# Kernel optimization log

Hardware: AMD Instinct MI355X
Metric: run time of the kernel (lower is better)

## Reference

```python
import jax, jax.numpy as jnp
import numpy as np

IN_CHS = 128
NUM_HEADS = 4
WIN = 7
N = WIN * WIN            # 49 tokens per window
QKDIM = 128              # ceil(in_chs/num_groups/num_heads)*num_heads
HEAD_DIM = QKDIM // NUM_HEADS
SCALE = HEAD_DIM ** -0.5
B = 4096                 # batch * num_windows


def _relative_position_index(win_h, win_w):
    coords = np.stack(np.meshgrid(np.arange(win_h), np.arange(win_w), indexing='ij'))  # [2,h,w]
    cf = coords.reshape(2, -1)                      # [2, N]
    rc = (cf[:, :, None] - cf[:, None, :]).transpose(1, 2, 0).astype(np.int64)  # [N,N,2]
    rc[:, :, 0] += win_h - 1
    rc[:, :, 1] += win_w - 1
    rc[:, :, 0] *= 2 * win_w - 1
    return rc.sum(-1)                               # [N, N]


def setup_inputs() -> dict:
    key = jax.random.key(0)
    ks = jax.random.split(key, 8)
    x = jax.random.normal(ks[0], (B, N, IN_CHS), dtype=jnp.float32)
    qk_w = jax.random.normal(ks[1], (2 * QKDIM, IN_CHS), dtype=jnp.float32) * 0.02
    qk_b = jnp.zeros((2 * QKDIM,), dtype=jnp.float32)
    v_w = jax.random.normal(ks[2], (IN_CHS, IN_CHS), dtype=jnp.float32) * 0.02
    v_b = jnp.zeros((IN_CHS,), dtype=jnp.float32)
    proj_w = jax.random.normal(ks[3], (IN_CHS, IN_CHS), dtype=jnp.float32) * 0.02
    proj_b = jnp.zeros((IN_CHS,), dtype=jnp.float32)
    bias_table = jax.random.normal(ks[4], ((2 * WIN - 1) * (2 * WIN - 1), NUM_HEADS), dtype=jnp.float32) * 0.02
    rel_idx = jnp.asarray(_relative_position_index(WIN, WIN))  # [N,N] int64
    return {"x": x, "qk_w": qk_w, "qk_b": qk_b, "v_w": v_w, "v_b": v_b,
            "proj_w": proj_w, "proj_b": proj_b, "bias_table": bias_table,
            "rel_idx": rel_idx}


def reference(x, qk_w, qk_b, v_w, v_b, proj_w, proj_b, bias_table, rel_idx):
    Bn, Nn, C = x.shape
    # fused q/k projection: [B,N,2*qkdim] -> q,k each [B,H,N,d]
    qk = (x @ qk_w.T + qk_b).reshape(Bn, Nn, 2, NUM_HEADS, HEAD_DIM)
    q = qk[:, :, 0].transpose(0, 2, 1, 3)
    k = qk[:, :, 1].transpose(0, 2, 1, 3)
    v = (x @ v_w.T + v_b).reshape(Bn, Nn, NUM_HEADS, -1).transpose(0, 2, 1, 3)
    # windowed QK^T with gathered relative-position bias
    attn = jnp.einsum('bhnd,bhmd->bhnm', q * SCALE, k)
    bias = bias_table[rel_idx.reshape(-1)].reshape(Nn, Nn, NUM_HEADS).transpose(2, 0, 1)
    attn = jax.nn.softmax(attn + bias[None], axis=-1)
    out = jnp.einsum('bhnm,bhmd->bhnd', attn, v).transpose(0, 2, 1, 3).reshape(Bn, Nn, -1)
    return out @ proj_w.T + proj_b
```

## Files before the change

### kernel.cpp

```cpp
#include <hip/hip_runtime.h>
#include <hip/hip_bf16.h>

typedef __attribute__((ext_vector_type(8))) __bf16 bf16x8;
typedef __attribute__((ext_vector_type(4))) short short4v;
typedef __attribute__((ext_vector_type(4))) float f32x4;

#define MFMA(a,b,c) __builtin_amdgcn_mfma_f32_16x16x32_bf16((a),(b),(c),0,0,0)
#define MFMA16(a,b,c) __builtin_amdgcn_mfma_f32_16x16x16bf16_1k((a),(b),(c),0,0,0)

#define XB 0u
#define QB 16384u
#define KB 32768u
#define VT 49152u

static __device__ __forceinline__ unsigned short f2u(float x) {
  return __builtin_bit_cast(unsigned short, static_cast<__bf16>(x));
}
static __device__ __forceinline__ unsigned long long pack4(float a, float b, float c, float d) {
  union { __bf16 h[4]; unsigned long long u; } z;
  z.h[0] = static_cast<__bf16>(a);
  z.h[1] = static_cast<__bf16>(b);
  z.h[2] = static_cast<__bf16>(c);
  z.h[3] = static_cast<__bf16>(d);
  return z.u;
}
static __device__ __forceinline__ unsigned long long pack4v(f32x4 v) {
  return pack4(v[0], v[1], v[2], v[3]);
}
static __device__ __forceinline__ short4v pack4s(float a, float b, float c, float d) {
  union { __bf16 h[4]; short4v s; } z;
  z.h[0] = static_cast<__bf16>(a);
  z.h[1] = static_cast<__bf16>(b);
  z.h[2] = static_cast<__bf16>(c);
  z.h[3] = static_cast<__bf16>(d);
  return z.s;
}
static __device__ __forceinline__ unsigned sw256(unsigned row, unsigned colb) {
  return (row << 8) + (colb ^ ((row & 7u) << 4));
}
static __device__ __forceinline__ unsigned sw128(unsigned row, unsigned colb) {
  return (row << 7) + (colb ^ ((row & 7u) << 4));
}

__global__ void rsa_prep(const float* __restrict__ qk_w, const float* __restrict__ v_w,
                         const float* __restrict__ proj_w, const float* __restrict__ bias_table,
                         unsigned short* __restrict__ wqk, unsigned short* __restrict__ wv,
                         unsigned short* __restrict__ wp, float* __restrict__ biasNN) {
  const float SCALE = 0.17677669529663687f;
  int t = blockIdx.x * blockDim.x + threadIdx.x;
  int stride = gridDim.x * blockDim.x;
  for (int i = t; i < 256 * 128; i += stride) {
    float v = qk_w[i];
    if (i < 128 * 128) v *= SCALE;
    wqk[i] = f2u(v);
  }
  for (int i = t; i < 128 * 128; i += stride) wv[i] = f2u(v_w[i]);
  for (int i = t; i < 128 * 128; i += stride) wp[i] = f2u(proj_w[i]);
  for (int i = t; i < 4 * 64 * 64; i += stride) {
    int h = i >> 12, r = (i >> 6) & 63, m = i & 63;
    float v = -1e9f;
    if (r < 49 && m < 49) {
      int ri = r / 7, rj = r - ri * 7, mi = m / 7, mj = m - mi * 7;
      int rel = (ri - mi + 6) * 13 + (rj - mj + 6);
      v = bias_table[rel * 4 + h];
    }
    biasNN[i] = v;
  }
}

__global__ __launch_bounds__(512, 4) void rsa_main(
    const float* __restrict__ x, const float* __restrict__ qk_bias,
    const float* __restrict__ v_bias, const float* __restrict__ proj_bias,
    const unsigned short* __restrict__ wqk, const unsigned short* __restrict__ wv,
    const unsigned short* __restrict__ wp, const float* __restrict__ biasNN,
    float* __restrict__ out) {
  __shared__ __align__(16) unsigned char LDS[65536];
  const int tid = threadIdx.x;
  const int w = tid >> 6;
  const int lane = tid & 63;
  const int c = lane & 15;
  const int g = lane >> 4;
  const int b = blockIdx.x;
  const float SCALE = 0.17677669529663687f;

  {
    const f32x4* xp = reinterpret_cast<const f32x4*>(x + (size_t)b * 6272);
    for (int i = tid; i < 1568; i += 512) {
      f32x4 v = xp[i];
      unsigned row = (unsigned)i >> 5, c4 = (unsigned)i & 31u;
      *reinterpret_cast<unsigned long long*>(LDS + XB + sw256(row, c4 * 8)) = pack4v(v);
    }
    for (int i = tid; i < 480; i += 512) {
      unsigned row = 49 + ((unsigned)i >> 5), c4 = (unsigned)i & 31u;
      *reinterpret_cast<unsigned long long*>(LDS + XB + sw256(row, c4 * 8)) = 0ull;
    }
  }
  __syncthreads();

  __builtin_amdgcn_s_setprio(1);
#pragma unroll
  for (int mi = 0; mi < 2; ++mi) {
    const int mt = w + 8 * mi;
    bf16x8 a[4];
    const unsigned short* wrow = wqk + (mt * 16 + c) * 128 + g * 8;
#pragma unroll
    for (int ks = 0; ks < 4; ++ks) a[ks] = *reinterpret_cast<const bf16x8*>(wrow + ks * 32);
    const int chout = mt * 16 + g * 4;
    f32x4 bias4 = *reinterpret_cast<const f32x4*>(qk_bias + chout);
    if (mi == 0) { bias4[0] *= SCALE; bias4[1] *= SCALE; bias4[2] *= SCALE; bias4[3] *= SCALE; }
#pragma unroll
    for (int nt = 0; nt < 4; ++nt) {
      f32x4 acc = {0.f, 0.f, 0.f, 0.f};
#pragma unroll
      for (int ks = 0; ks < 4; ++ks) {
        bf16x8 bf = *reinterpret_cast<const bf16x8*>(LDS + XB + sw256(nt * 16 + c, (ks * 32 + g * 8) * 2));
        acc = MFMA(a[ks], bf, acc);
      }
      const unsigned tok = nt * 16 + c;
      const unsigned colb = ((mt & 7) * 16 + g * 4) * 2;
      const unsigned base = (mi == 0) ? QB : KB;
      *reinterpret_cast<unsigned long long*>(LDS + base + sw256(tok, colb)) =
          pack4(acc[0] + bias4[0], acc[1] + bias4[1], acc[2] + bias4[2], acc[3] + bias4[3]);
    }
  }

  {
    const float vb = v_bias[w * 16 + c];
    bf16x8 bw[4];
    const unsigned short* wrow = wv + (w * 16 + c) * 128 + g * 8;
#pragma unroll
    for (int ks = 0; ks < 4; ++ks) bw[ks] = *reinterpret_cast<const bf16x8*>(wrow + ks * 32);
#pragma unroll
    for (int mt = 0; mt < 4; ++mt) {
      f32x4 acc = {0.f, 0.f, 0.f, 0.f};
#pragma unroll
      for (int ks = 0; ks < 4; ++ks) {
        bf16x8 af = *reinterpret_cast<const bf16x8*>(LDS + XB + sw256(mt * 16 + c, (ks * 32 + g * 8) * 2));
        acc = MFMA(af, bw[ks], acc);
      }
      const unsigned row = w * 16 + c;
      const unsigned colb = (mt * 16 + g * 4) * 2;
      *reinterpret_cast<unsigned long long*>(LDS + VT + sw128(row, colb)) =
          pack4(acc[0] + vb, acc[1] + vb, acc[2] + vb, acc[3] + vb);
    }
  }
  __builtin_amdgcn_s_setprio(0);
  __syncthreads();

  const int h = w >> 1;
  const int rt0 = (w & 1) * 2;

  f32x4 bb[2][4];
#pragma unroll
  for (int r2 = 0; r2 < 2; ++r2) {
    const int r = (rt0 + r2) * 16 + c;
    const float* bp = biasNN + ((h * 64 + r) << 6);
#pragma unroll
    for (int mt = 0; mt < 4; ++mt)
      bb[r2][mt] = *reinterpret_cast<const f32x4*>(bp + mt * 16 + g * 4);
  }

  f32x4 s[2][4];
  __builtin_amdgcn_s_setprio(1);
#pragma unroll
  for (int r2 = 0; r2 < 2; ++r2) {
    const int rt = rt0 + r2;
    bf16x8 qf = *reinterpret_cast<const bf16x8*>(LDS + QB + sw256(rt * 16 + c, h * 64 + g * 16));
#pragma unroll
    for (int mt = 0; mt < 4; ++mt) {
      bf16x8 kf = *reinterpret_cast<const bf16x8*>(LDS + KB + sw256(mt * 16 + c, h * 64 + g * 16));
      f32x4 z = {0.f, 0.f, 0.f, 0.f};
      s[r2][mt] = MFMA(kf, qf, z);
    }
  }
  __builtin_amdgcn_s_setprio(0);

  short4v pk[2][4];
#pragma unroll
  for (int r2 = 0; r2 < 2; ++r2) {
    float v[16];
    float sum = 0.f;
#pragma unroll
    for (int mt = 0; mt < 4; ++mt) {
#pragma unroll
      for (int j = 0; j < 4; ++j) {
        v[mt * 4 + j] = __expf(s[r2][mt][j] + bb[r2][mt][j]);
        sum += v[mt * 4 + j];
      }
    }
    sum += __shfl_xor(sum, 16);
    sum += __shfl_xor(sum, 32);
    const float inv = (sum > 0.f) ? 1.0f / sum : 0.f;
#pragma unroll
    for (int mt = 0; mt < 4; ++mt)
      pk[r2][mt] = pack4s(v[mt * 4] * inv, v[mt * 4 + 1] * inv,
                          v[mt * 4 + 2] * inv, v[mt * 4 + 3] * inv);
  }

  f32x4 od[2][2];
  {
    short4v vfrag[2][4];
#pragma unroll
    for (int ct2 = 0; ct2 < 2; ++ct2)
#pragma unroll
      for (int ks = 0; ks < 4; ++ks)
        vfrag[ct2][ks] = *reinterpret_cast<const short4v*>(
            LDS + VT + sw128((h * 2 + ct2) * 16 + c, (ks * 16 + g * 4) * 2));
    __builtin_amdgcn_s_setprio(1);
#pragma unroll
    for (int ct2 = 0; ct2 < 2; ++ct2)
#pragma unroll
      for (int r2 = 0; r2 < 2; ++r2) {
        f32x4 acc = {0.f, 0.f, 0.f, 0.f};
#pragma unroll
        for (int ks = 0; ks < 4; ++ks) acc = MFMA16(vfrag[ct2][ks], pk[r2][ks], acc);
        od[ct2][r2] = acc;
      }
    __builtin_amdgcn_s_setprio(0);
  }

  bf16x8 ap[4];
  {
    const unsigned short* wrow = wp + (w * 16 + c) * 128 + g * 8;
#pragma unroll
    for (int ks = 0; ks < 4; ++ks) ap[ks] = *reinterpret_cast<const bf16x8*>(wrow + ks * 32);
  }
  f32x4 pb4 = *reinterpret_cast<const f32x4*>(proj_bias + w * 16 + g * 4);

#pragma unroll
  for (int ct2 = 0; ct2 < 2; ++ct2)
#pragma unroll
    for (int r2 = 0; r2 < 2; ++r2) {
      const int r = (rt0 + r2) * 16 + c;
      *reinterpret_cast<unsigned long long*>(
          LDS + XB + sw256(r, ((h * 2 + ct2) * 16 + g * 4) * 2)) = pack4v(od[ct2][r2]);
    }
  __syncthreads();

  {
    __builtin_amdgcn_s_setprio(1);
#pragma unroll
    for (int nt = 0; nt < 4; ++nt) {
      f32x4 acc = {0.f, 0.f, 0.f, 0.f};
#pragma unroll
      for (int ks = 0; ks < 4; ++ks) {
        bf16x8 bf = *reinterpret_cast<const bf16x8*>(LDS + XB + sw256(nt * 16 + c, (ks * 32 + g * 8) * 2));
        acc = MFMA(ap[ks], bf, acc);
      }
      const int tok = nt * 16 + c;
      if (tok < 49) {
        f32x4 o = {acc[0] + pb4[0], acc[1] + pb4[1], acc[2] + pb4[2], acc[3] + pb4[3]};
        *reinterpret_cast<f32x4*>(out + ((size_t)b * 49 + tok) * 128 + w * 16 + g * 4) = o;
      }
    }
    __builtin_amdgcn_s_setprio(0);
  }
}

extern "C" void kernel_launch(void* const* d_in, const int* in_sizes, int n_in,
                              void* d_out, int out_size, void* d_ws, size_t ws_size,
                              hipStream_t stream) {
  const float* x          = (const float*)d_in[0];
  const float* qk_w       = (const float*)d_in[1];
  const float* qk_b       = (const float*)d_in[2];
  const float* v_w        = (const float*)d_in[3];
  const float* v_b        = (const float*)d_in[4];
  const float* proj_w     = (const float*)d_in[5];
  const float* proj_b     = (const float*)d_in[6];
  const float* bias_table = (const float*)d_in[7];
  float* out = (float*)d_out;

  unsigned short* wqk = (unsigned short*)d_ws;
  unsigned short* wv  = wqk + 256 * 128;
  unsigned short* wp  = wv + 128 * 128;
  float* biasNN = (float*)((char*)d_ws + 131072);

  const int B = in_sizes[0] / (49 * 128);

  rsa_prep<<<dim3(128), dim3(512), 0, stream>>>(qk_w, v_w, proj_w, bias_table, wqk, wv, wp, biasNN);
  rsa_main<<<dim3(B), dim3(512), 0, stream>>>(x, qk_b, v_b, proj_b, wqk, wv, wp, biasNN, out);
}
```

Before: 119.2 us.

## Process four windows per block with register-prefetched next-window input

Measured after the change: 171.2 us. 1.44x slower.

```diff
diff --git a/kernel.cpp b/kernel.cpp
--- a/kernel.cpp
+++ b/kernel.cpp
@@ -12,6 +12,8 @@
 #define QB 16384u
 #define KB 32768u
 #define VT 49152u
+#define OB 65536u
+#define NW 4
 
 static __device__ __forceinline__ unsigned short f2u(float x) {
   return __builtin_bit_cast(unsigned short, static_cast<__bf16>(x));
@@ -41,17 +43,23 @@
 static __device__ __forceinline__ unsigned sw128(unsigned row, unsigned colb) {
   return (row << 7) + (colb ^ ((row & 7u) << 4));
 }
+template <typename T>
+static __device__ __forceinline__ const T* opq(const T* p) {
+  asm volatile("" : "+s"(p));
+  return p;
+}
 
 __global__ void rsa_prep(const float* __restrict__ qk_w, const float* __restrict__ v_w,
                          const float* __restrict__ proj_w, const float* __restrict__ bias_table,
                          unsigned short* __restrict__ wqk, unsigned short* __restrict__ wv,
                          unsigned short* __restrict__ wp, float* __restrict__ biasNN) {
-  const float SCALE = 0.17677669529663687f;
+  const float QSCALE = 0.17677669529663687f * 1.4426950408889634f;
+  const float LOG2E = 1.4426950408889634f;
   int t = blockIdx.x * blockDim.x + threadIdx.x;
   int stride = gridDim.x * blockDim.x;
   for (int i = t; i < 256 * 128; i += stride) {
     float v = qk_w[i];
-    if (i < 128 * 128) v *= SCALE;
+    if (i < 128 * 128) v *= QSCALE;
     wqk[i] = f2u(v);
   }
   for (int i = t; i < 128 * 128; i += stride) wv[i] = f2u(v_w[i]);
@@ -62,7 +70,7 @@
     if (r < 49 && m < 49) {
       int ri = r / 7, rj = r - ri * 7, mi = m / 7, mj = m - mi * 7;
       int rel = (ri - mi + 6) * 13 + (rj - mj + 6);
-      v = bias_table[rel * 4 + h];
+      v = bias_table[rel * 4 + h] * LOG2E;
     }
     biasNN[i] = v;
   }
@@ -73,187 +81,209 @@
     const float* __restrict__ v_bias, const float* __restrict__ proj_bias,
     const unsigned short* __restrict__ wqk, const unsigned short* __restrict__ wv,
     const unsigned short* __restrict__ wp, const float* __restrict__ biasNN,
-    float* __restrict__ out) {
-  __shared__ __align__(16) unsigned char LDS[65536];
+    float* __restrict__ out, int Btot) {
+  __shared__ __align__(16) unsigned char LDS[81920];
   const int tid = threadIdx.x;
   const int w = tid >> 6;
   const int lane = tid & 63;
   const int c = lane & 15;
   const int g = lane >> 4;
-  const int b = blockIdx.x;
-  const float SCALE = 0.17677669529663687f;
-
-  {
-    const f32x4* xp = reinterpret_cast<const f32x4*>(x + (size_t)b * 6272);
-    for (int i = tid; i < 1568; i += 512) {
-      f32x4 v = xp[i];
-      unsigned row = (unsigned)i >> 5, c4 = (unsigned)i & 31u;
-      *reinterpret_cast<unsigned long long*>(LDS + XB + sw256(row, c4 * 8)) = pack4v(v);
-    }
-    for (int i = tid; i < 480; i += 512) {
-      unsigned row = 49 + ((unsigned)i >> 5), c4 = (unsigned)i & 31u;
-      *reinterpret_cast<unsigned long long*>(LDS + XB + sw256(row, c4 * 8)) = 0ull;
-    }
-  }
-  __syncthreads();
-
-  __builtin_amdgcn_s_setprio(1);
-#pragma unroll
-  for (int mi = 0; mi < 2; ++mi) {
-    const int mt = w + 8 * mi;
-    bf16x8 a[4];
-    const unsigned short* wrow = wqk + (mt * 16 + c) * 128 + g * 8;
-#pragma unroll
-    for (int ks = 0; ks < 4; ++ks) a[ks] = *reinterpret_cast<const bf16x8*>(wrow + ks * 32);
-    const int chout = mt * 16 + g * 4;
-    f32x4 bias4 = *reinterpret_cast<const f32x4*>(qk_bias + chout);
-    if (mi == 0) { bias4[0] *= SCALE; bias4[1] *= SCALE; bias4[2] *= SCALE; bias4[3] *= SCALE; }
-#pragma unroll
-    for (int nt = 0; nt < 4; ++nt) {
-      f32x4 acc = {0.f, 0.f, 0.f, 0.f};
-#pragma unroll
-      for (int ks = 0; ks < 4; ++ks) {
-        bf16x8 bf = *reinterpret_cast<const bf16x8*>(LDS + XB + sw256(nt * 16 + c, (ks * 32 + g * 8) * 2));
-        acc = MFMA(a[ks], bf, acc);
-      }
-      const unsigned tok = nt * 16 + c;
-      const unsigned colb = ((mt & 7) * 16 + g * 4) * 2;
-      const unsigned base = (mi == 0) ? QB : KB;
-      *reinterpret_cast<unsigned long long*>(LDS + base + sw256(tok, colb)) =
-          pack4(acc[0] + bias4[0], acc[1] + bias4[1], acc[2] + bias4[2], acc[3] + bias4[3]);
-    }
-  }
-
-  {
-    const float vb = v_bias[w * 16 + c];
-    bf16x8 bw[4];
-    const unsigned short* wrow = wv + (w * 16 + c) * 128 + g * 8;
-#pragma unroll
-    for (int ks = 0; ks < 4; ++ks) bw[ks] = *reinterpret_cast<const bf16x8*>(wrow + ks * 32);
-#pragma unroll
-    for (int mt = 0; mt < 4; ++mt) {
-      f32x4 acc = {0.f, 0.f, 0.f, 0.f};
-#pragma unroll
-      for (int ks = 0; ks < 4; ++ks) {
-        bf16x8 af = *reinterpret_cast<const bf16x8*>(LDS + XB + sw256(mt * 16 + c, (ks * 32 + g * 8) * 2));
-        acc = MFMA(af, bw[ks], acc);
-      }
-      const unsigned row = w * 16 + c;
-      const unsigned colb = (mt * 16 + g * 4) * 2;
-      *reinterpret_cast<unsigned long long*>(LDS + VT + sw128(row, colb)) =
-          pack4(acc[0] + vb, acc[1] + vb, acc[2] + vb, acc[3] + vb);
-    }
-  }
-  __builtin_amdgcn_s_setprio(0);
-  __syncthreads();
-
   const int h = w >> 1;
   const int rt0 = (w & 1) * 2;
-
-  f32x4 bb[2][4];
-#pragma unroll
-  for (int r2 = 0; r2 < 2; ++r2) {
-    const int r = (rt0 + r2) * 16 + c;
-    const float* bp = biasNN + ((h * 64 + r) << 6);
-#pragma unroll
-    for (int mt = 0; mt < 4; ++mt)
-      bb[r2][mt] = *reinterpret_cast<const f32x4*>(bp + mt * 16 + g * 4);
-  }
-
-  f32x4 s[2][4];
-  __builtin_amdgcn_s_setprio(1);
-#pragma unroll
-  for (int r2 = 0; r2 < 2; ++r2) {
-    const int rt = rt0 + r2;
-    bf16x8 qf = *reinterpret_cast<const bf16x8*>(LDS + QB + sw256(rt * 16 + c, h * 64 + g * 16));
-#pragma unroll
-    for (int mt = 0; mt < 4; ++mt) {
-      bf16x8 kf = *reinterpret_cast<const bf16x8*>(LDS + KB + sw256(mt * 16 + c, h * 64 + g * 16));
-      f32x4 z = {0.f, 0.f, 0.f, 0.f};
-      s[r2][mt] = MFMA(kf, qf, z);
-    }
-  }
-  __builtin_amdgcn_s_setprio(0);
-
-  short4v pk[2][4];
-#pragma unroll
-  for (int r2 = 0; r2 < 2; ++r2) {
-    float v[16];
-    float sum = 0.f;
-#pragma unroll
-    for (int mt = 0; mt < 4; ++mt) {
-#pragma unroll
-      for (int j = 0; j < 4; ++j) {
-        v[mt * 4 + j] = __expf(s[r2][mt][j] + bb[r2][mt][j]);
-        sum += v[mt * 4 + j];
-      }
-    }
-    sum += __shfl_xor(sum, 16);
-    sum += __shfl_xor(sum, 32);
-    const float inv = (sum > 0.f) ? 1.0f / sum : 0.f;
-#pragma unroll
-    for (int mt = 0; mt < 4; ++mt)
-      pk[r2][mt] = pack4s(v[mt * 4] * inv, v[mt * 4 + 1] * inv,
-                          v[mt * 4 + 2] * inv, v[mt * 4 + 3] * inv);
-  }
-
-  f32x4 od[2][2];
-  {
-    short4v vfrag[2][4];
+  const float QBSCALE = 0.17677669529663687f * 1.4426950408889634f;
+
+  const int b0 = blockIdx.x * NW;
+  if (b0 >= Btot) return;
+  const int nw = (Btot - b0 < NW) ? (Btot - b0) : NW;
+
+#pragma unroll 1
+  for (int i = 0; i < nw; ++i) {
+    const int b = b0 + i;
+
+    if (i == 0) {
+      const f32x4* xp = reinterpret_cast<const f32x4*>(x + (size_t)b * 6272);
+      for (int t2 = tid; t2 < 1568; t2 += 512) {
+        f32x4 v = xp[t2];
+        unsigned row = (unsigned)t2 >> 5, c4 = (unsigned)t2 & 31u;
+        *reinterpret_cast<unsigned long long*>(LDS + XB + sw256(row, c4 * 8)) = pack4v(v);
+      }
+      for (int t2 = tid; t2 < 480; t2 += 512) {
+        unsigned row = 49 + ((unsigned)t2 >> 5), c4 = (unsigned)t2 & 31u;
+        *reinterpret_cast<unsigned long long*>(LDS + XB + sw256(row, c4 * 8)) = 0ull;
+      }
+    }
+    __syncthreads();
+
+    __builtin_amdgcn_s_setprio(1);
+#pragma unroll
+    for (int mi = 0; mi < 2; ++mi) {
+      const int mt = w + 8 * mi;
+      bf16x8 a[4];
+      const unsigned short* wrow = opq(wqk) + (mt * 16 + c) * 128 + g * 8;
+#pragma unroll
+      for (int ks = 0; ks < 4; ++ks) a[ks] = *reinterpret_cast<const bf16x8*>(wrow + ks * 32);
+      f32x4 bias4 = *reinterpret_cast<const f32x4*>(opq(qk_bias) + mt * 16 + g * 4);
+      if (mi == 0) { bias4[0] *= QBSCALE; bias4[1] *= QBSCALE; bias4[2] *= QBSCALE; bias4[3] *= QBSCALE; }
+#pragma unroll
+      for (int nt = 0; nt < 4; ++nt) {
+        f32x4 acc = {0.f, 0.f, 0.f, 0.f};
+#pragma unroll
+        for (int ks = 0; ks < 4; ++ks) {
+          bf16x8 bf = *reinterpret_cast<const bf16x8*>(LDS + XB + sw256(nt * 16 + c, (ks * 32 + g * 8) * 2));
+          acc = MFMA(a[ks], bf, acc);
+        }
+        const unsigned tok = nt * 16 + c;
+        const unsigned colb = ((mt & 7) * 16 + g * 4) * 2;
+        const unsigned base = (mi == 0) ? QB : KB;
+        *reinterpret_cast<unsigned long long*>(LDS + base + sw256(tok, colb)) =
+            pack4(acc[0] + bias4[0], acc[1] + bias4[1], acc[2] + bias4[2], acc[3] + bias4[3]);
+      }
+    }
+
+    {
+      const float vb = opq(v_bias)[w * 16 + c];
+      bf16x8 bw[4];
+      const unsigned short* wrow = opq(wv) + (w * 16 + c) * 128 + g * 8;
+#pragma unroll
+      for (int ks = 0; ks < 4; ++ks) bw[ks] = *reinterpret_cast<const bf16x8*>(wrow + ks * 32);
+#pragma unroll
+      for (int mt = 0; mt < 4; ++mt) {
+        f32x4 acc = {0.f, 0.f, 0.f, 0.f};
+#pragma unroll
+        for (int ks = 0; ks < 4; ++ks) {
+          bf16x8 af = *reinterpret_cast<const bf16x8*>(LDS + XB + sw256(mt * 16 + c, (ks * 32 + g * 8) * 2));
+          acc = MFMA(af, bw[ks], acc);
+        }
+        *reinterpret_cast<unsigned long long*>(LDS + VT + sw128(w * 16 + c, (mt * 16 + g * 4) * 2)) =
+            pack4(acc[0] + vb, acc[1] + vb, acc[2] + vb, acc[3] + vb);
+      }
+    }
+    __builtin_amdgcn_s_setprio(0);
+    __syncthreads();
+
+    f32x4 bb[2][4];
+#pragma unroll
+    for (int r2 = 0; r2 < 2; ++r2) {
+      const float* bp = opq(biasNN) + ((h * 64 + (rt0 + r2) * 16 + c) << 6);
+#pragma unroll
+      for (int mt = 0; mt < 4; ++mt)
+        bb[r2][mt] = *reinterpret_cast<const f32x4*>(bp + mt * 16 + g * 4);
+    }
+
+    f32x4 s[2][4];
+    __builtin_amdgcn_s_setprio(1);
+#pragma unroll
+    for (int r2 = 0; r2 < 2; ++r2) {
+      bf16x8 qf = *reinterpret_cast<const bf16x8*>(LDS + QB + sw256((rt0 + r2) * 16 + c, h * 64 + g * 16));
+#pragma unroll
+      for (int mt = 0; mt < 4; ++mt) {
+        bf16x8 kf = *reinterpret_cast<const bf16x8*>(LDS + KB + sw256(mt * 16 + c, h * 64 + g * 16));
+        f32x4 z = {0.f, 0.f, 0.f, 0.f};
+        s[r2][mt] = MFMA(kf, qf, z);
+      }
+    }
+    __builtin_amdgcn_s_setprio(0);
+
+    short4v pk[2][4];
+#pragma unroll
+    for (int r2 = 0; r2 < 2; ++r2) {
+      float v[16];
+      float sum = 0.f;
+#pragma unroll
+      for (int mt = 0; mt < 4; ++mt) {
+#pragma unroll
+        for (int j = 0; j < 4; ++j) {
+          v[mt * 4 + j] = exp2f(s[r2][mt][j] + bb[r2][mt][j]);
+          sum += v[mt * 4 + j];
+        }
+      }
+      sum += __shfl_xor(sum, 16);
+      sum += __shfl_xor(sum, 32);
+      const float inv = (sum > 0.f) ? 1.0f / sum : 0.f;
+#pragma unroll
+      for (int mt = 0; mt < 4; ++mt)
+        pk[r2][mt] = pack4s(v[mt * 4] * inv, v[mt * 4 + 1] * inv,
+                            v[mt * 4 + 2] * inv, v[mt * 4 + 3] * inv);
+    }
+
+    f32x4 xr0, xr1, xr2, xr3;
+    if (i + 1 < nw) {
+      const f32x4* xp = reinterpret_cast<const f32x4*>(x + (size_t)(b + 1) * 6272);
+      xr0 = xp[tid];
+      xr1 = xp[tid + 512];
+      xr2 = xp[tid + 1024];
+      xr3 = (tid < 32) ? xp[tid + 1536] : f32x4{0.f, 0.f, 0.f, 0.f};
+    }
+
+    f32x4 od[2][2];
+    {
+      short4v vfrag[2][4];
+#pragma unroll
+      for (int ct2 = 0; ct2 < 2; ++ct2)
+#pragma unroll
+        for (int ks = 0; ks < 4; ++ks)
+          vfrag[ct2][ks] = *reinterpret_cast<const short4v*>(
+              LDS + VT + sw128((h * 2 + ct2) * 16 + c, (ks * 16 + g * 4) * 2));
+      __builtin_amdgcn_s_setprio(1);
+#pragma unroll
+      for (int ct2 = 0; ct2 < 2; ++ct2)
+#pragma unroll
+        for (int r2 = 0; r2 < 2; ++r2) {
+          f32x4 acc = {0.f, 0.f, 0.f, 0.f};
+#pragma unroll
+          for (int ks = 0; ks < 4; ++ks) acc = MFMA16(vfrag[ct2][ks], pk[r2][ks], acc);
+          od[ct2][r2] = acc;
+        }
+      __builtin_amdgcn_s_setprio(0);
+    }
+
+    bf16x8 ap[4];
+    {
+      const unsigned short* wrow = opq(wp) + (w * 16 + c) * 128 + g * 8;
+#pragma unroll
+      for (int ks = 0; ks < 4; ++ks) ap[ks] = *reinterpret_cast<const bf16x8*>(wrow + ks * 32);
+    }
+    f32x4 pb4 = *reinterpret_cast<const f32x4*>(opq(proj_bias) + w * 16 + g * 4);
+
 #pragma unroll
     for (int ct2 = 0; ct2 < 2; ++ct2)
 #pragma unroll
-      for (int ks = 0; ks < 4; ++ks)
-        vfrag[ct2][ks] = *reinterpret_cast<const short4v*>(
-            LDS + VT + sw128((h * 2 + ct2) * 16 + c, (ks * 16 + g * 4) * 2));
-    __builtin_amdgcn_s_setprio(1);
-#pragma unroll
-    for (int ct2 = 0; ct2 < 2; ++ct2)
-#pragma unroll
       for (int r2 = 0; r2 < 2; ++r2) {
+        const int r = (rt0 + r2) * 16 + c;
+        *reinterpret_cast<unsigned long long*>(
+            LDS + OB + sw256(r, ((h * 2 + ct2) * 16 + g * 4) * 2)) = pack4v(od[ct2][r2]);
+      }
+
+    if (i + 1 < nw) {
+      unsigned idx0 = (unsigned)tid;
+      *reinterpret_cast<unsigned long long*>(LDS + XB + sw256(idx0 >> 5, (idx0 & 31u) * 8)) = pack4v(xr0);
+      unsigned idx1 = (unsigned)tid + 512u;
+      *reinterpret_cast<unsigned long long*>(LDS + XB + sw256(idx1 >> 5, (idx1 & 31u) * 8)) = pack4v(xr1);
+      unsigned idx2 = (unsigned)tid + 1024u;
+      *reinterpret_cast<unsigned long long*>(LDS + XB + sw256(idx2 >> 5, (idx2 & 31u) * 8)) = pack4v(xr2);
+      unsigned idx3 = (unsigned)tid + 1536u;
+      *reinterpret_cast<unsigned long long*>(LDS + XB + sw256(idx3 >> 5, (idx3 & 31u) * 8)) = pack4v(xr3);
+    }
+    __syncthreads();
+
+    {
+      __builtin_amdgcn_s_setprio(1);
+#pragma unroll
+      for (int nt = 0; nt < 4; ++nt) {
         f32x4 acc = {0.f, 0.f, 0.f, 0.f};
 #pragma unroll
-        for (int ks = 0; ks < 4; ++ks) acc = MFMA16(vfrag[ct2][ks], pk[r2][ks], acc);
-        od[ct2][r2] = acc;
-      }
-    __builtin_amdgcn_s_setprio(0);
-  }
-
-  bf16x8 ap[4];
-  {
-    const unsigned short* wrow = wp + (w * 16 + c) * 128 + g * 8;
-#pragma unroll
-    for (int ks = 0; ks < 4; ++ks) ap[ks] = *reinterpret_cast<const bf16x8*>(wrow + ks * 32);
-  }
-  f32x4 pb4 = *reinterpret_cast<const f32x4*>(proj_bias + w * 16 + g * 4);
-
-#pragma unroll
-  for (int ct2 = 0; ct2 < 2; ++ct2)
-#pragma unroll
-    for (int r2 = 0; r2 < 2; ++r2) {
-      const int r = (rt0 + r2) * 16 + c;
-      *reinterpret_cast<unsigned long long*>(
-          LDS + XB + sw256(r, ((h * 2 + ct2) * 16 + g * 4) * 2)) = pack4v(od[ct2][r2]);
-    }
-  __syncthreads();
-
-  {
-    __builtin_amdgcn_s_setprio(1);
-#pragma unroll
-    for (int nt = 0; nt < 4; ++nt) {
-      f32x4 acc = {0.f, 0.f, 0.f, 0.f};
-#pragma unroll
-      for (int ks = 0; ks < 4; ++ks) {
-        bf16x8 bf = *reinterpret_cast<const bf16x8*>(LDS + XB + sw256(nt * 16 + c, (ks * 32 + g * 8) * 2));
-        acc = MFMA(ap[ks], bf, acc);
-      }
-      const int tok = nt * 16 + c;
-      if (tok < 49) {
-        f32x4 o = {acc[0] + pb4[0], acc[1] + pb4[1], acc[2] + pb4[2], acc[3] + pb4[3]};
-        *reinterpret_cast<f32x4*>(out + ((size_t)b * 49 + tok) * 128 + w * 16 + g * 4) = o;
-      }
-    }
-    __builtin_amdgcn_s_setprio(0);
+        for (int ks = 0; ks < 4; ++ks) {
+          bf16x8 bf = *reinterpret_cast<const bf16x8*>(LDS + OB + sw256(nt * 16 + c, (ks * 32 + g * 8) * 2));
+          acc = MFMA(ap[ks], bf, acc);
+        }
+        const int tok = nt * 16 + c;
+        if (tok < 49) {
+          f32x4 o = {acc[0] + pb4[0], acc[1] + pb4[1], acc[2] + pb4[2], acc[3] + pb4[3]};
+          *reinterpret_cast<f32x4*>(out + ((size_t)b * 49 + tok) * 128 + w * 16 + g * 4) = o;
+        }
+      }
+      __builtin_amdgcn_s_setprio(0);
+    }
   }
 }
 
@@ -276,7 +306,8 @@
   float* biasNN = (float*)((char*)d_ws + 131072);
 
   const int B = in_sizes[0] / (49 * 128);
+  const int grid = (B + NW - 1) / NW;
 
   rsa_prep<<<dim3(128), dim3(512), 0, stream>>>(qk_w, v_w, proj_w, bias_table, wqk, wv, wp, biasNN);
-  rsa_main<<<dim3(B), dim3(512), 0, stream>>>(x, qk_b, v_b, proj_b, wqk, wv, wp, biasNN, out);
-}
+  rsa_main<<<dim3(grid), dim3(512), 0, stream>>>(x, qk_b, v_b, proj_b, wqk, wv, wp, biasNN, out, B);
+}
```
